# Kernel optimization log

Measured on AMD Instinct MI355X. Metric: run time of the kernel, lower is better.

The kernel has to match this reference:

```python
import jax, jax.numpy as jnp
import numpy as np

B, FEAT, Q, L, H_ENC, H_DEC = 256, 64, 16, 2, 128, 256


def _apply_1q(state, U, q):
    # state: [B, 2,2,...,2] (Q qubit axes); U: [B,2,2] complex64
    s = jnp.moveaxis(state, 1 + q, 1)
    shp = s.shape
    s2 = s.reshape(shp[0], 2, -1)
    s2 = jnp.einsum('bij,bjr->bir', U, s2)
    return jnp.moveaxis(s2.reshape(shp), 1, 1 + q)


def _apply_cnot(state, c, t):
    # flip target axis on the control=1 slice
    c0 = jnp.take(state, 0, axis=1 + c)
    c1 = jnp.take(state, 1, axis=1 + c)
    t_ax = 1 + t if t < c else t  # target axis index after removing control axis
    c1 = jnp.flip(c1, axis=t_ax)
    return jnp.stack([c0, c1], axis=1 + c)


def _u3(theta, phi, lam):
    # combined Rz(lam) @ Ry(phi) @ Rx(theta); inputs [B] -> [B,2,2] complex64
    j = jnp.complex64(1j)
    ct, st = jnp.cos(theta / 2), jnp.sin(theta / 2)
    cp, sp = jnp.cos(phi / 2), jnp.sin(phi / 2)
    Rx = jnp.stack([jnp.stack([ct + 0j, -j * st], -1),
                    jnp.stack([-j * st, ct + 0j], -1)], -2)
    Ry = jnp.stack([jnp.stack([cp + 0j, -sp + 0j], -1),
                    jnp.stack([sp + 0j, cp + 0j], -1)], -2)
    em, ep = jnp.exp(-j * lam / 2), jnp.exp(j * lam / 2)
    zero = jnp.zeros_like(em)
    Rz = jnp.stack([jnp.stack([em, zero], -1),
                    jnp.stack([zero, ep], -1)], -2)
    return jnp.einsum('bij,bjk,bkl->bil', Rz, Ry, Rx).astype(jnp.complex64)


def setup_inputs() -> dict:
    key = jax.random.key(0)
    ks = jax.random.split(key, 6)

    def xavier(k, shape):
        lim = float(np.sqrt(6.0 / (shape[0] + shape[1])))
        return jax.random.uniform(k, shape, jnp.float32, -lim, lim)

    return {
        'x': jax.random.normal(ks[0], (B, FEAT), jnp.float32),
        'W1': xavier(ks[1], (FEAT, H_ENC)), 'b1': jnp.zeros((H_ENC,), jnp.float32),
        'W2': xavier(ks[2], (H_ENC, L * Q * 3)), 'b2': jnp.zeros((L * Q * 3,), jnp.float32),
        'scaling': jnp.ones((Q,), jnp.float32),
        'Wd1': xavier(ks[3], (2 ** Q, H_DEC)), 'bd1': jnp.zeros((H_DEC,), jnp.float32),
        'Wd2': xavier(ks[4], (H_DEC, FEAT)), 'bd2': jnp.zeros((FEAT,), jnp.float32),
    }


def reference(x, W1, b1, W2, b2, scaling, Wd1, bd1, Wd2, bd2):
    batch = x.shape[0]
    nq = scaling.shape[0]
    nl = W2.shape[1] // (nq * 3)
    # classical encoder -> quantum rotation angles
    h = jax.nn.relu(x @ W1 + b1)
    p = jnp.tanh(h @ W2 + b2).reshape(batch, nl, nq, 3)
    p = p * scaling[None, None, :, None] * jnp.pi  # theta/phi/lambda scaled by pi
    # batched statevector simulation, |0...0> init
    state = jnp.zeros((batch, 2 ** nq), jnp.complex64).at[:, 0].set(1.0)
    state = state.reshape((batch,) + (2,) * nq)
    for l in range(nl):
        for q in range(nq):
            U = _u3(p[:, l, q, 0], p[:, l, q, 1], p[:, l, q, 2])
            state = _apply_1q(state, U, q)
        if l < nl - 1:
            for q in range(nq - 1):
                state = _apply_cnot(state, q, q + 1)
            state = _apply_cnot(state, nq - 1, 0)
    probs = (jnp.real(state) ** 2 + jnp.imag(state) ** 2).reshape(batch, -1)
    # classical decoder
    out = jax.nn.relu(jax.nn.relu(probs @ Wd1 + bd1) @ Wd2 + bd2)
    return out
```

## Files before the change

kernel.cpp:

```cpp
#include <hip/hip_runtime.h>
#include <hip/hip_fp16.h>

#define PI_F 3.14159265358979323846f

typedef __attribute__((ext_vector_type(8))) _Float16 f16x8;
typedef __attribute__((ext_vector_type(16))) float f32x16;
typedef __attribute__((ext_vector_type(2))) float v2f;

__device__ __forceinline__ v2f pfma(v2f a, v2f b, v2f c) {
    return __builtin_elementwise_fma(a, b, c);
}
__device__ __forceinline__ v2f vswap(v2f a) { return __builtin_shufflevector(a, a, 1, 0); }
__device__ __forceinline__ v2f vsplat(float x) { v2f r; r.x = x; r.y = x; return r; }
__device__ __forceinline__ v2f mkc(v2f u) { v2f r; r.x = -u.y; r.y = u.y; return r; }
__device__ __forceinline__ v2f cmul(v2f a, v2f b) {
    return pfma(mkc(a), vswap(b), vsplat(a.x) * b);
}

__device__ __forceinline__ unsigned f2bf_rn(float x) {
    unsigned u = __float_as_uint(x);
    return (u + 0x7fffu + ((u >> 16) & 1u)) >> 16;
}

union H8 { int4 i4; f16x8 v; };

__device__ __forceinline__ void gll16(const void* g, void* l) {
    __builtin_amdgcn_global_load_lds(
        (const __attribute__((address_space(1))) void*)g,
        (__attribute__((address_space(3))) void*)l, 16, 0, 0);
}

union PreLds {
    struct {
        float xr[64]; float h[128]; float ang[96];
        v2f vL[32];
        v2f uL[64];
        _Float16 lR[256*8];
        _Float16 lL[512*8];
    } e;
    _Float16 wt[64][260];
};

__global__ __launch_bounds__(256) void k_pre(
        const float* __restrict__ x, const float* __restrict__ W1,
        const float* __restrict__ b1, const float* __restrict__ W2,
        const float* __restrict__ b2, const float* __restrict__ scaling,
        const float* __restrict__ Wd1, _Float16* __restrict__ Wt,
        _Float16* __restrict__ A) {
    __shared__ PreLds lds;
    const int t = threadIdx.x;
    if (blockIdx.x >= 256) {
        const int cb = blockIdx.x - 256;
        const int kb = (cb >> 2) * 256;
        const int nb = (cb & 3) * 64;
        #pragma unroll
        for (int it = 0; it < 16; ++it) {
            int idx = t + it*256;
            int kr = idx >> 4;
            int nc = (idx & 15) * 4;
            float4 w = *(const float4*)(Wd1 + (size_t)(kb + kr)*256 + nb + nc);
            lds.wt[nc+0][kr] = (_Float16)(w.x * 64.f);
            lds.wt[nc+1][kr] = (_Float16)(w.y * 64.f);
            lds.wt[nc+2][kr] = (_Float16)(w.z * 64.f);
            lds.wt[nc+3][kr] = (_Float16)(w.w * 64.f);
        }
        __syncthreads();
        const int wv = t >> 6, ln = t & 63;
        const int u = ln & 31;
        #pragma unroll
        for (int r = 0; r < 8; ++r) {
            int n = r*8 + wv*2 + (ln >> 5);
            int4 hh = *(const int4*)&lds.wt[n][u*8];
            *(int4*)(Wt + ((size_t)(nb + n) << 16) + kb + u*8) = hh;
        }
        return;
    }
    const int b = blockIdx.x;
    if (t < 64) lds.e.xr[t] = x[b*64 + t];
    __syncthreads();
    if (t < 128) {
        float acc = b1[t];
        #pragma unroll 8
        for (int f = 0; f < 64; ++f) acc = fmaf(lds.e.xr[f], W1[f*128 + t], acc);
        lds.e.h[t] = fmaxf(acc, 0.f);
    }
    __syncthreads();
    if (t < 96) {
        float acc = b2[t];
        #pragma unroll 8
        for (int f = 0; f < 128; ++f) acc = fmaf(lds.e.h[f], W2[f*96 + t], acc);
        int q = (t/3) & 15;
        lds.e.ang[t] = tanhf(acc) * scaling[q] * PI_F;
    }
    __syncthreads();
    if (t < 32) {
        int l = t >> 4, q = t & 15;
        const float* a = lds.e.ang + l*48 + q*3;
        float st, ct, sp, cp, sl, cl;
        sincosf(a[0]*0.5f, &st, &ct);
        sincosf(a[1]*0.5f, &sp, &cp);
        sincosf(a[2]*0.5f, &sl, &cl);
        float2 A00 = make_float2( cp*ct,  sp*st);
        float2 A01 = make_float2(-sp*ct, -cp*st);
        float2 A10 = make_float2( sp*ct, -cp*st);
        float2 A11 = make_float2( cp*ct, -sp*st);
        float2 e0 = make_float2(cl, -sl), e1 = make_float2(cl, sl);
        v2f r00; r00.x = e0.x*A00.x - e0.y*A00.y; r00.y = e0.x*A00.y + e0.y*A00.x;
        v2f r01; r01.x = e0.x*A01.x - e0.y*A01.y; r01.y = e0.x*A01.y + e0.y*A01.x;
        v2f r10; r10.x = e1.x*A10.x - e1.y*A10.y; r10.y = e1.x*A10.y + e1.y*A10.x;
        v2f r11; r11.x = e1.x*A11.x - e1.y*A11.y; r11.y = e1.x*A11.y + e1.y*A11.x;
        if (l == 0) {
            lds.e.vL[q*2 + 0] = r00;
            lds.e.vL[q*2 + 1] = r10;
        } else {
            lds.e.uL[q*4 + 0] = r00; lds.e.uL[q*4 + 1] = r01;
            lds.e.uL[q*4 + 2] = r10; lds.e.uL[q*4 + 3] = r11;
        }
    }
    __syncthreads();
    #define AP(p, s) lds.e.vL[(15-(p))*2 + (s)]
    #define GG(p, zv, yv) lds.e.uL[(15-(p))*4 + (zv)*2 + (yv)]
    const float SL = 32.f;
    v2f Lg[2][2];
    {
        int z0 = t & 1, z1 = (t >> 1) & 1;
        #pragma unroll
        for (int g = 0; g < 2; ++g)
            #pragma unroll
            for (int y = 0; y < 2; ++y)
                Lg[g][y] = cmul(cmul(GG(0, z0, g), AP(0, g ^ y)), GG(1, z1, y));
        #pragma unroll
        for (int p = 2; p <= 7; ++p) {
            int zp = (t >> p) & 1;
            #pragma unroll
            for (int g = 0; g < 2; ++g) {
                v2f s0 = cmul(Lg[g][0], AP(p-1, 0)) + cmul(Lg[g][1], AP(p-1, 1));
                v2f s1 = cmul(Lg[g][0], AP(p-1, 1)) + cmul(Lg[g][1], AP(p-1, 0));
                Lg[g][0] = cmul(s0, GG(p, zp, 0));
                Lg[g][1] = cmul(s1, GG(p, zp, 1));
            }
        }
    }
    v2f Rg[2][2];
    {
        int z15 = (t >> 7) & 1;
        #pragma unroll
        for (int g = 0; g < 2; ++g)
            #pragma unroll
            for (int y14 = 0; y14 < 2; ++y14)
                Rg[g][y14] = cmul(cmul(AP(14, y14 ^ g),     AP(15, g)),     GG(15, z15, 0))
                           + cmul(cmul(AP(14, y14 ^ 1 ^ g), AP(15, 1 ^ g)), GG(15, z15, 1));
        #pragma unroll
        for (int p = 14; p >= 8; --p) {
            int zp = (t >> (p - 8)) & 1;
            #pragma unroll
            for (int g = 0; g < 2; ++g) {
                v2f t0 = cmul(GG(p, zp, 0), Rg[g][0]);
                v2f t1 = cmul(GG(p, zp, 1), Rg[g][1]);
                v2f n0 = cmul(AP(p-1, 0), t0) + cmul(AP(p-1, 1), t1);
                v2f n1 = cmul(AP(p-1, 1), t0) + cmul(AP(p-1, 0), t1);
                Rg[g][0] = n0; Rg[g][1] = n1;
            }
        }
    }
    #undef AP
    #undef GG
    {
        float lre[4] = {Lg[0][0].x, Lg[0][1].x, Lg[1][0].x, Lg[1][1].x};
        float lim[4] = {Lg[0][0].y, Lg[0][1].y, Lg[1][0].y, Lg[1][1].y};
        float rre[4] = {Rg[0][0].x, Rg[0][1].x, Rg[1][0].x, Rg[1][1].x};
        float rim[4] = {Rg[0][0].y, Rg[0][1].y, Rg[1][0].y, Rg[1][1].y};
        H8 hre, him, hr;
        #pragma unroll
        for (int k = 0; k < 4; ++k) {
            hre.v[k]   = (_Float16)(SL * lre[k]);
            hre.v[4+k] = (_Float16)(-SL * lim[k]);
            him.v[k]   = (_Float16)(SL * lim[k]);
            him.v[4+k] = (_Float16)(SL * lre[k]);
            hr.v[k]    = (_Float16)(SL * rre[k]);
            hr.v[4+k]  = (_Float16)(SL * rim[k]);
        }
        *(int4*)&lds.e.lR[t*8]         = hr.i4;
        *(int4*)&lds.e.lL[t*8]         = hre.i4;
        *(int4*)&lds.e.lL[(256+t)*8]   = him.i4;
    }
    __syncthreads();
    {
        const int wave = t >> 6, lane = t & 63, h2 = lane >> 5, l32 = lane & 31;
        f16x8 zf = {};
        _Float16* Aout = A + ((size_t)b << 16);
        #pragma unroll
        for (int mt2 = 0; mt2 < 2; ++mt2) {
            const int zh0 = (wave*2 + mt2)*32;
            f16x8 af = h2 ? zf : *(const f16x8*)&lds.e.lR[(zh0 + l32)*8];
            #pragma unroll
            for (int j = 0; j < 8; ++j) {
                f16x8 bre = h2 ? zf : *(const f16x8*)&lds.e.lL[(j*32 + l32)*8];
                f16x8 bim = h2 ? zf : *(const f16x8*)&lds.e.lL[(256 + j*32 + l32)*8];
                f32x16 zc = {};
                f32x16 dre = __builtin_amdgcn_mfma_f32_32x32x16_f16(af, bre, zc, 0, 0, 0);
                f32x16 dim = __builtin_amdgcn_mfma_f32_32x32x16_f16(af, bim, zc, 0, 0, 0);
                #pragma unroll
                for (int q = 0; q < 16; ++q) {
                    float p = fmaf(dre[q], dre[q], dim[q]*dim[q]) * 0.00390625f;
                    int row = zh0 + 4*h2 + (q & 3) + 8*(q >> 2);
                    Aout[row*256 + j*32 + l32] = (_Float16)p;
                }
            }
        }
    }
}

__global__ __launch_bounds__(256, 4) void k_gemm(
        const _Float16* __restrict__ A, const _Float16* __restrict__ Bt,
        unsigned short* __restrict__ partial) {
    __shared__ _Float16 lA[128*64];
    __shared__ _Float16 lB[128*64];
    const int ks = blockIdx.x, nt = blockIdx.y, mt = blockIdx.z;
    const int k0 = ks*256, n0 = nt*128, m0 = mt*128;
    const int tid = threadIdx.x, wave = tid >> 6, lane = tid & 63;
    const int mw = wave >> 1, nw = wave & 1;
    const int h = lane >> 5, l32 = lane & 31;
    f32x16 acc[2][2] = {};
    for (int s = 0; s < 4; ++s) {
        const int kb = k0 + s*64;
        #pragma unroll
        for (int i = 0; i < 4; ++i) {
            int ia = wave*4 + i;
            int r = ia*8 + (lane >> 3);
            int cch = (lane & 7) ^ (r & 7);
            gll16(A  + (size_t)(m0 + r)*65536 + kb + cch*8, &lA[ia*512]);
            gll16(Bt + (size_t)(n0 + r)*65536 + kb + cch*8, &lB[ia*512]);
        }
        __syncthreads();
        #pragma unroll
        for (int kk = 0; kk < 4; ++kk) {
            const int ch = kk*2 + h;
            f16x8 af[2], bf[2];
            #pragma unroll
            for (int xx = 0; xx < 2; ++xx) {
                int rA = mw*64 + xx*32 + l32;
                af[xx] = *(const f16x8*)&lA[rA*64 + ((ch ^ (rA & 7)) << 3)];
                int rB = nw*64 + xx*32 + l32;
                bf[xx] = *(const f16x8*)&lB[rB*64 + ((ch ^ (rB & 7)) << 3)];
            }
            #pragma unroll
            for (int i = 0; i < 2; ++i)
                #pragma unroll
                for (int jj = 0; jj < 2; ++jj)
                    acc[i][jj] = __builtin_amdgcn_mfma_f32_32x32x16_f16(af[i], bf[jj], acc[i][jj], 0, 0, 0);
        }
        __syncthreads();
    }
    unsigned short* pp = partial + (size_t)ks*65536;
    #pragma unroll
    for (int i = 0; i < 2; ++i) {
        #pragma unroll
        for (int jj = 0; jj < 2; ++jj) {
            int n = n0 + nw*64 + jj*32 + l32;
            int mb = m0 + mw*64 + i*32 + 4*h;
            #pragma unroll
            for (int q = 0; q < 16; ++q) {
                int m = mb + (q & 3) + 8*(q >> 2);
                pp[m*256 + n] = (unsigned short)f2bf_rn(acc[i][jj][q]);
            }
        }
    }
}

__global__ __launch_bounds__(256) void k_red(
        const unsigned short* __restrict__ partial, float* __restrict__ partial2) {
    const int m = blockIdx.x & 255, g = blockIdx.x >> 8;
    const int t = threadIdx.x;
    const unsigned short* p = partial + (size_t)(g*32)*65536 + m*256 + t;
    float s = 0.f;
    #pragma unroll 8
    for (int kc = 0; kc < 32; ++kc)
        s += __uint_as_float(((unsigned)p[(size_t)kc*65536]) << 16);
    partial2[((size_t)g*256 + m)*256 + t] = s;
}

__global__ __launch_bounds__(256) void k_final(
        const float* __restrict__ partial2, const float* __restrict__ bd1,
        const float* __restrict__ Wd2, const float* __restrict__ bd2,
        float* __restrict__ out) {
    __shared__ float row[256];
    const int m = blockIdx.x, t = threadIdx.x;
    {
        float s = 0.f;
        #pragma unroll
        for (int g = 0; g < 8; ++g)
            s += partial2[((size_t)g*256 + m)*256 + t];
        const float SC = 1.f / 262144.f;
        row[t] = fmaxf(fmaf(s, SC, bd1[t]), 0.f);
    }
    __syncthreads();
    if (t < 64) {
        float o = bd2[t];
        #pragma unroll 8
        for (int n = 0; n < 256; ++n) o = fmaf(row[n], Wd2[n*64 + t], o);
        out[m*64 + t] = fmaxf(o, 0.f);
    }
}

extern "C" void kernel_launch(void* const* d_in, const int* in_sizes, int n_in,
                              void* d_out, int out_size, void* d_ws, size_t ws_size,
                              hipStream_t stream) {
    const float* x       = (const float*)d_in[0];
    const float* W1      = (const float*)d_in[1];
    const float* b1      = (const float*)d_in[2];
    const float* W2      = (const float*)d_in[3];
    const float* b2      = (const float*)d_in[4];
    const float* scaling = (const float*)d_in[5];
    const float* Wd1     = (const float*)d_in[6];
    const float* bd1     = (const float*)d_in[7];
    const float* Wd2     = (const float*)d_in[8];
    const float* bd2     = (const float*)d_in[9];
    float* out = (float*)d_out;

    char* ws = (char*)d_ws;
    const size_t MB = 1024*1024;
    _Float16* A  = (_Float16*)(ws + 4*MB);
    _Float16* Wt = (_Float16*)(ws + 36*MB);
    unsigned short* partial = (unsigned short*)(ws + 68*MB);
    float* partial2 = (float*)(ws + 100*MB);

    hipLaunchKernelGGL(k_pre, dim3(1280), dim3(256), 0, stream,
                       x, W1, b1, W2, b2, scaling, Wd1, Wt, A);
    hipLaunchKernelGGL(k_gemm, dim3(256, 2, 2), dim3(256), 0, stream, A, Wt, partial);
    hipLaunchKernelGGL(k_red, dim3(2048), dim3(256), 0, stream, partial, partial2);
    hipLaunchKernelGGL(k_final, dim3(256), dim3(256), 0, stream,
                       partial2, bd1, Wd2, bd2, out);
}
```

Measured before the change: 172.4 us.

## Halve GEMM split-K count, swizzle block order, and pack Wd1 transpose writes

The split-K GEMM now gives each block 512 of K instead of 256, so it runs 512 blocks instead of 1024. A 1D grid is remapped so that blocks sharing a K-slice across the 4 M/N tiles are adjacent, which should help L2 reuse. This halves the bf16 partial buffer, so the reduction reads 16 partials instead of 32. The Wd1 transpose in k_pre now converts two K rows at once into half2 and stores 32-bit words to LDS with a padded stride, reading rows back as two uint2 loads. The intent is to cut partial-buffer traffic and LDS store count, at the cost of fewer GEMM blocks to hide latency.

```diff
diff --git a/kernel.cpp b/kernel.cpp
--- a/kernel.cpp
+++ b/kernel.cpp
@@ -53,16 +53,23 @@
         const int cb = blockIdx.x - 256;
         const int kb = (cb >> 2) * 256;
         const int nb = (cb & 3) * 64;
-        #pragma unroll
-        for (int it = 0; it < 16; ++it) {
+        unsigned* wtw = (unsigned*)&lds.wt[0][0];
+        #pragma unroll
+        for (int it = 0; it < 8; ++it) {
             int idx = t + it*256;
-            int kr = idx >> 4;
-            int nc = (idx & 15) * 4;
-            float4 w = *(const float4*)(Wd1 + (size_t)(kb + kr)*256 + nb + nc);
-            lds.wt[nc+0][kr] = (_Float16)(w.x * 64.f);
-            lds.wt[nc+1][kr] = (_Float16)(w.y * 64.f);
-            lds.wt[nc+2][kr] = (_Float16)(w.z * 64.f);
-            lds.wt[nc+3][kr] = (_Float16)(w.w * 64.f);
+            int kr2 = idx >> 4;
+            int nc4 = (idx & 15) * 4;
+            const float* src = Wd1 + (size_t)(kb + 2*kr2)*256 + nb + nc4;
+            float4 w0 = *(const float4*)src;
+            float4 w1 = *(const float4*)(src + 256);
+            #pragma unroll
+            for (int j = 0; j < 4; ++j) {
+                float a0 = (j==0?w0.x:j==1?w0.y:j==2?w0.z:w0.w) * 64.f;
+                float a1 = (j==0?w1.x:j==1?w1.y:j==2?w1.z:w1.w) * 64.f;
+                __half2 hh = __floats2half2_rn(a0, a1);
+                unsigned u; __builtin_memcpy(&u, &hh, 4);
+                wtw[(nc4 + j)*130 + kr2] = u;
+            }
         }
         __syncthreads();
         const int wv = t >> 6, ln = t & 63;
@@ -70,7 +77,9 @@
         #pragma unroll
         for (int r = 0; r < 8; ++r) {
             int n = r*8 + wv*2 + (ln >> 5);
-            int4 hh = *(const int4*)&lds.wt[n][u*8];
+            uint2 lo = *(const uint2*)&lds.wt[n][u*8];
+            uint2 hi = *(const uint2*)&lds.wt[n][u*8 + 4];
+            int4 hh = make_int4((int)lo.x, (int)lo.y, (int)hi.x, (int)hi.y);
             *(int4*)(Wt + ((size_t)(nb + n) << 16) + kb + u*8) = hh;
         }
         return;
@@ -216,13 +225,16 @@
         unsigned short* __restrict__ partial) {
     __shared__ _Float16 lA[128*64];
     __shared__ _Float16 lB[128*64];
-    const int ks = blockIdx.x, nt = blockIdx.y, mt = blockIdx.z;
-    const int k0 = ks*256, n0 = nt*128, m0 = mt*128;
+    const int id = blockIdx.x;
+    const int ks = (id & 7) | ((id >> 5) << 3);
+    const int p  = (id >> 3) & 3;
+    const int nt = p >> 1, mt = p & 1;
+    const int k0 = ks*512, n0 = nt*128, m0 = mt*128;
     const int tid = threadIdx.x, wave = tid >> 6, lane = tid & 63;
     const int mw = wave >> 1, nw = wave & 1;
     const int h = lane >> 5, l32 = lane & 31;
     f32x16 acc[2][2] = {};
-    for (int s = 0; s < 4; ++s) {
+    for (int s = 0; s < 8; ++s) {
         const int kb = k0 + s*64;
         #pragma unroll
         for (int i = 0; i < 4; ++i) {
@@ -272,10 +284,10 @@
         const unsigned short* __restrict__ partial, float* __restrict__ partial2) {
     const int m = blockIdx.x & 255, g = blockIdx.x >> 8;
     const int t = threadIdx.x;
-    const unsigned short* p = partial + (size_t)(g*32)*65536 + m*256 + t;
+    const unsigned short* p = partial + (size_t)(g*16)*65536 + m*256 + t;
     float s = 0.f;
-    #pragma unroll 8
-    for (int kc = 0; kc < 32; ++kc)
+    #pragma unroll 16
+    for (int kc = 0; kc < 16; ++kc)
         s += __uint_as_float(((unsigned)p[(size_t)kc*65536]) << 16);
     partial2[((size_t)g*256 + m)*256 + t] = s;
 }
@@ -323,11 +335,11 @@
     _Float16* A  = (_Float16*)(ws + 4*MB);
     _Float16* Wt = (_Float16*)(ws + 36*MB);
     unsigned short* partial = (unsigned short*)(ws + 68*MB);
-    float* partial2 = (float*)(ws + 100*MB);
+    float* partial2 = (float*)(ws + 84*MB);
 
     hipLaunchKernelGGL(k_pre, dim3(1280), dim3(256), 0, stream,
                        x, W1, b1, W2, b2, scaling, Wd1, Wt, A);
-    hipLaunchKernelGGL(k_gemm, dim3(256, 2, 2), dim3(256), 0, stream, A, Wt, partial);
+    hipLaunchKernelGGL(k_gemm, dim3(512), dim3(256), 0, stream, A, Wt, partial);
     hipLaunchKernelGGL(k_red, dim3(2048), dim3(256), 0, stream, partial, partial2);
     hipLaunchKernelGGL(k_final, dim3(256), dim3(256), 0, stream,
                        partial2, bd1, Wd2, bd2, out);
```

Measured after the change: 170.1 us. About the same (-1.3%).
